# Performance work log

Hardware: AMD Instinct MI355X
Metric: run time of the kernel (lower is better)

## Reference

```python
import jax, jax.numpy as jnp
import numpy as np

NUM_GRAPHS = 512

def gcn_conv(x, src, dst, W, b, n):
    # x: [N, Fin], W: [Fin, Fout]. PyG GCNConv: add self loops, symmetric norm.
    h = x @ W  # [N, Fout]
    loop = jnp.arange(n)
    s = jnp.concatenate([src, loop])
    d = jnp.concatenate([dst, loop])
    ones = jnp.ones(s.shape[0], dtype=h.dtype)
    deg = jax.ops.segment_sum(ones, d, num_segments=n)  # includes self loop -> >= 1
    dinv = jax.lax.rsqrt(deg)
    norm = dinv[s] * dinv[d]  # [E+N]
    msg = h[s] * norm[:, None]  # gather + scale (memory-bound)
    out = jax.ops.segment_sum(msg, d, num_segments=n)
    return out + b

def setup_inputs() -> dict:
    key = jax.random.key(0)
    ks = jax.random.split(key, 10)
    N, E, F, H, O, EF = 100000, 1600000, 128, 128, 1, 16
    x = jax.random.normal(ks[0], (N, F), dtype=jnp.float32)
    edge_index = jax.random.randint(ks[1], (2, E), 0, N)
    edge_attr = jax.random.normal(ks[2], (E, EF), dtype=jnp.float32)
    batch = jnp.sort(jax.random.randint(ks[3], (N,), 0, NUM_GRAPHS))
    s1 = 1.0 / np.sqrt(F)
    s2 = 1.0 / np.sqrt(H)
    W1 = jax.random.uniform(ks[4], (F, H), jnp.float32, -s1, s1)
    b1 = jnp.zeros((H,), jnp.float32)
    W2 = jax.random.uniform(ks[5], (H, H), jnp.float32, -s2, s2)
    b2 = jnp.zeros((H,), jnp.float32)
    Wl = jax.random.uniform(ks[6], (H, O), jnp.float32, -s2, s2)
    bl = jnp.zeros((O,), jnp.float32)
    return {"x": x, "edge_index": edge_index, "edge_attr": edge_attr, "batch": batch,
            "W1": W1, "b1": b1, "W2": W2, "b2": b2, "Wl": Wl, "bl": bl}

def reference(x, edge_index, edge_attr, batch, W1, b1, W2, b2, Wl, bl):
    n = x.shape[0]
    src, dst = edge_index[0], edge_index[1]
    h = jax.nn.relu(gcn_conv(x, src, dst, W1, b1, n))
    h = gcn_conv(h, src, dst, W2, b2, n)
    # global mean pool by graph id
    summed = jax.ops.segment_sum(h, batch, num_segments=NUM_GRAPHS)  # [G, H]
    counts = jax.ops.segment_sum(jnp.ones((n,), h.dtype), batch, num_segments=NUM_GRAPHS)
    pooled = summed / jnp.maximum(counts, 1.0)[:, None]
    return pooled @ Wl + bl  # [G, 1]
```

## Files before the change

kernel.cpp:

```cpp
#include <hip/hip_runtime.h>


typedef __attribute__((ext_vector_type(8))) short short8;
typedef __attribute__((ext_vector_type(4))) float f32x4;

#define CHUNK 4096
#define RW    128
#define SCAP  6144
#define JCAP  512

__device__ __forceinline__ unsigned short bf16r(float f) {
    unsigned u = __float_as_uint(f);
    u += 0x7FFFu + ((u >> 16) & 1u);
    return (unsigned short)(u >> 16);
}

__device__ __forceinline__ float bff(unsigned short u) {
    return __uint_as_float((unsigned)u << 16);
}

__global__ void k_w1pack(const float* __restrict__ W1, unsigned short* __restrict__ w1p,
                         const float* __restrict__ W2, const float* __restrict__ Wl,
                         float* __restrict__ w2l) {
    if (blockIdx.x == 64) {
        int i = threadIdx.x;
        if (i < 128) {
            float s = 0.0f;
            for (int j = 0; j < 128; ++j) s = fmaf(W2[i * 128 + j], Wl[j], s);
            w2l[i] = s;
        }
        return;
    }
    int idx = blockIdx.x * 256 + threadIdx.x;
    int k = idx >> 7, n = idx & 127;
    w1p[((k >> 3) * 128 + n) * 8 + (k & 7)] = bf16r(W1[idx]);
}

__global__ __launch_bounds__(256) void k_part(
    const int* __restrict__ src, const int* __restrict__ dst,
    int* __restrict__ part, int* __restrict__ off_t, int* __restrict__ cnt_t,
    int E, int nchunks, int NR)
{
    __shared__ int stage[CHUNK];
    __shared__ int lcnt[1024];
    __shared__ int lscan[1024];
    int tid = threadIdx.x;
    int j = blockIdx.x;
    int base = j * CHUNK;

#pragma unroll
    for (int k = 0; k < 4; ++k) lcnt[tid + k * 256] = 0;
    __syncthreads();

    int mye[16], myr[16];
#pragma unroll
    for (int k = 0; k < 16; ++k) {
        int e = base + tid + (k << 8);
        bool ok = e < E;
        int s = ok ? src[e] : 0;
        int d = ok ? dst[e] : 0;
        int r = -1;
        if (ok) {
            r = d >> 7;
            atomicAdd(&lcnt[r], 1);
        }
        mye[k] = (s << 7) | (d & 127);
        myr[k] = r;
    }
    __syncthreads();

    int* pa = lcnt;
    int* pb = lscan;
    for (int off = 1; off < 1024; off <<= 1) {
#pragma unroll
        for (int k = 0; k < 4; ++k) {
            int idx = tid + k * 256;
            int v = pa[idx];
            if (idx >= off) v += pa[idx - off];
            pb[idx] = v;
        }
        __syncthreads();
        int* tmp = pa; pa = pb; pb = tmp;
    }
    for (int i = tid; i < NR; i += 256) {
        int incl = pa[i];
        int excl = (i == 0) ? 0 : pa[i - 1];
        pb[i] = excl;
        off_t[(size_t)i * nchunks + j] = excl;
        cnt_t[(size_t)i * nchunks + j] = incl - excl;
    }
    __syncthreads();

#pragma unroll
    for (int k = 0; k < 16; ++k) {
        if (myr[k] >= 0) {
            int p = atomicAdd(&pb[myr[k]], 1);
            stage[p] = mye[k];
        }
    }
    __syncthreads();

    int valid = E - base; if (valid > CHUNK) valid = CHUNK;
    for (int i = tid; i < valid; i += 256)
        part[(size_t)base + i] = stage[i];
}

__global__ __launch_bounds__(64) void k_rtot(
    const int* __restrict__ cnt_t, int* __restrict__ rtot, int nchunks)
{
    int r = blockIdx.x;
    int lane = threadIdx.x;
    const int* row = cnt_t + (size_t)r * nchunks;
    int s = 0;
    for (int j = lane; j < nchunks; j += 64) s += row[j];
#pragma unroll
    for (int off = 32; off > 0; off >>= 1) s += __shfl_xor(s, off);
    if (lane == 0) rtot[r] = s;
}

__global__ __launch_bounds__(1024) void k_rbase(
    const int* __restrict__ rtot, int* __restrict__ rbase, int NR)
{
    __shared__ int a1[1024], a2[1024];
    int tid = threadIdx.x;
    a1[tid] = (tid < NR) ? rtot[tid] : 0;
    __syncthreads();
    int* pa = a1; int* pb = a2;
    for (int off = 1; off < 1024; off <<= 1) {
        int v = pa[tid];
        if (tid >= off) v += pa[tid - off];
        pb[tid] = v;
        __syncthreads();
        int* tmp = pa; pa = pb; pb = tmp;
    }
    if (tid < NR) rbase[tid] = (tid == 0) ? 0 : pa[tid - 1];
    if (tid == 0) rbase[NR] = pa[NR >= 1 ? NR - 1 : 0];
}

__global__ __launch_bounds__(256) void k_rscat(
    const int* __restrict__ part, const int* __restrict__ off_t,
    const int* __restrict__ cnt_t, const int* __restrict__ rbase,
    int* __restrict__ srt, int* __restrict__ rp, float* __restrict__ dinv,
    int nchunks, int N, int E)
{
    __shared__ int stage[SCAP];
    __shared__ int jbase[JCAP];
    __shared__ int hist[RW], lcur[RW], s1[RW], s2[RW];
    __shared__ int cursor;
    int r = blockIdx.x;
    int tid = threadIdx.x;
    int d0 = r << 7;
    int width = N - d0; if (width > RW) width = RW;
    if (tid < RW) hist[tid] = 0;
    if (tid == 0) cursor = 0;
    __syncthreads();

    const int* orow = off_t + (size_t)r * nchunks;
    const int* crow = cnt_t + (size_t)r * nchunks;

    for (int j = tid; j < nchunks; j += 256) {
        int c = crow[j];
        if (c == 0) { if (j < JCAP) jbase[j] = 0; continue; }
        int b = (j < JCAP) ? atomicAdd(&cursor, c) : SCAP;
        if (j < JCAP) jbase[j] = b;
        const int* pp = part + (size_t)j * CHUNK + orow[j];
        for (int e = 0; e < c; ++e) {
            int ed = pp[e];
            int pos = b + e;
            if (pos < SCAP) stage[pos] = ed;
            atomicAdd(&hist[ed & 127], 1);
        }
    }
    __syncthreads();
    int total = cursor;

    if (tid < RW) s1[tid] = hist[tid];
    __syncthreads();
    int* pa = s1; int* pb = s2;
    for (int off = 1; off < RW; off <<= 1) {
        if (tid < RW) {
            int v = pa[tid];
            if (tid >= off) v += pa[tid - off];
            pb[tid] = v;
        }
        __syncthreads();
        int* tmp = pa; pa = pb; pb = tmp;
    }
    if (tid < width) {
        int excl = (tid == 0) ? 0 : pa[tid - 1];
        int start = rbase[r] + excl;
        rp[d0 + tid] = start;
        lcur[tid] = start;
        dinv[d0 + tid] = 1.0f / sqrtf((float)hist[tid] + 1.0f);
    }
    if (r == 0 && tid == 0) rp[N] = E;
    __syncthreads();

    int lim = total < SCAP ? total : SCAP;
    for (int i = tid; i < lim; i += 256) {
        int ed = stage[i];
        int pos = atomicAdd(&lcur[ed & 127], 1);
        srt[pos] = ed >> 7;
    }
    if (total > SCAP || nchunks > JCAP) {
        for (int j = tid; j < nchunks; j += 256) {
            int c = crow[j];
            if (c == 0) continue;
            int e0 = 0;
            if (j < JCAP) {
                int b = jbase[j];
                e0 = SCAP - b;
                if (e0 < 0) e0 = 0;
                if (e0 >= c) continue;
            }
            const int* pp = part + (size_t)j * CHUNK + orow[j];
            for (int e = e0; e < c; ++e) {
                int ed = pp[e];
                int pos = atomicAdd(&lcur[ed & 127], 1);
                srt[pos] = ed >> 7;
            }
        }
    }
}

__global__ __launch_bounds__(256) void k_mm_mfma(
    const float* __restrict__ A, const unsigned short* __restrict__ w1p,
    const float* __restrict__ dinv, unsigned short* __restrict__ C, int N)
{
    __shared__ unsigned short w1s[16384];
    int tid = threadIdx.x;
    {
        const uint4* s = (const uint4*)w1p;
        uint4* d = (uint4*)w1s;
#pragma unroll
        for (int i = 0; i < 8; ++i) d[tid + i * 256] = s[tid + i * 256];
    }
    __syncthreads();

    int w = tid >> 6, lane = tid & 63;
    int m = lane & 15, quad = lane >> 4;
    int r0 = blockIdx.x * 128 + w * 32;

    f32x4 acc[2][8];
#pragma unroll
    for (int rg = 0; rg < 2; ++rg)
#pragma unroll
        for (int cg = 0; cg < 8; ++cg) {
            f32x4 z = {0.0f, 0.0f, 0.0f, 0.0f};
            acc[rg][cg] = z;
        }

#pragma unroll
    for (int ks = 0; ks < 4; ++ks) {
        int k0 = ks * 32 + quad * 8;
        short8 a[2];
#pragma unroll
        for (int rg = 0; rg < 2; ++rg) {
            int r = r0 + rg * 16 + m;
            if (r > N - 1) r = N - 1;
            const float* ap = A + (size_t)r * 128 + k0;
            float4 v0 = *(const float4*)ap;
            float4 v1 = *(const float4*)(ap + 4);
            short8 av;
            av[0] = (short)bf16r(v0.x); av[1] = (short)bf16r(v0.y);
            av[2] = (short)bf16r(v0.z); av[3] = (short)bf16r(v0.w);
            av[4] = (short)bf16r(v1.x); av[5] = (short)bf16r(v1.y);
            av[6] = (short)bf16r(v1.z); av[7] = (short)bf16r(v1.w);
            a[rg] = av;
        }
        int kc = ks * 4 + quad;
#pragma unroll
        for (int cg = 0; cg < 8; ++cg) {
            const short8* bp = (const short8*)&w1s[((size_t)kc * 128 + cg * 16 + m) * 8];
            short8 b = *bp;
            acc[0][cg] = __builtin_amdgcn_mfma_f32_16x16x32_bf16(a[0], b, acc[0][cg], 0, 0, 0);
            acc[1][cg] = __builtin_amdgcn_mfma_f32_16x16x32_bf16(a[1], b, acc[1][cg], 0, 0, 0);
        }
    }

#pragma unroll
    for (int rg = 0; rg < 2; ++rg) {
        int rbase2 = r0 + rg * 16 + quad * 4;
#pragma unroll
        for (int reg = 0; reg < 4; ++reg) {
            int r = rbase2 + reg;
            if (r < N) {
                float s = dinv[r];
#pragma unroll
                for (int cg = 0; cg < 8; ++cg)
                    C[(size_t)r * 128 + cg * 16 + m] = bf16r(acc[rg][cg][reg] * s);
            }
        }
    }
}

__global__ __launch_bounds__(256) void k_agg1(
    const unsigned short* __restrict__ t, const float* __restrict__ dinv,
    const int* __restrict__ rp, const int* __restrict__ srt,
    const float* __restrict__ b1, const float* __restrict__ w2l,
    float* __restrict__ q, int N)
{
    __shared__ int shi[4][64];
    int wave = threadIdx.x >> 6;
    int lane = threadIdx.x & 63;
    int node = blockIdx.x * 4 + wave;
    if (node >= N) return;
    int s0 = rp[node], s1 = rp[node + 1];
    int deg = s1 - s0;
    int vdeg = deg < 63 ? deg : 63;

    int idx = N;
    if (lane < vdeg) idx = srt[s0 + lane];
    else if (lane == vdeg) idx = node;
    shi[wave][lane] = idx;
    const int* shw = shi[wave];

    int r4 = lane >> 4;
    int c = lane & 15;
    const unsigned short* tc = t + c * 8;

    float a[8];
#pragma unroll
    for (int k = 0; k < 8; ++k) a[k] = 0.0f;

    int nrows = vdeg + 1;
    int nquads = (nrows + 3) >> 2;
    int p = 0;
    do {
        short8 v[8];
#pragma unroll
        for (int j = 0; j < 8; ++j) {
            int id = shw[((p + j) << 2) + r4];
            v[j] = *(const short8*)(tc + (size_t)id * 128);
        }
#pragma unroll
        for (int j = 0; j < 8; ++j)
#pragma unroll
            for (int k = 0; k < 8; ++k)
                a[k] += bff((unsigned short)v[j][k]);
        p += 8;
    } while (p < nquads);

    if (deg > 63) {
        for (int e = s0 + 63; e < s1; ++e) {
            int id = srt[e];
            short8 v = *(const short8*)(tc + (size_t)id * 128);
            if (r4 == 0)
#pragma unroll
                for (int k = 0; k < 8; ++k)
                    a[k] += bff((unsigned short)v[k]);
        }
    }

#pragma unroll
    for (int k = 0; k < 8; ++k) {
        a[k] += __shfl_xor(a[k], 16);
        a[k] += __shfl_xor(a[k], 32);
    }

    float di = dinv[node];
    float4 b0 = *(const float4*)(b1 + c * 8);
    float4 b4 = *(const float4*)(b1 + c * 8 + 4);
    float4 w0 = *(const float4*)(w2l + c * 8);
    float4 w4 = *(const float4*)(w2l + c * 8 + 4);
    float pr = 0.0f;
    pr += fmaxf(fmaf(a[0], di, b0.x), 0.0f) * w0.x;
    pr += fmaxf(fmaf(a[1], di, b0.y), 0.0f) * w0.y;
    pr += fmaxf(fmaf(a[2], di, b0.z), 0.0f) * w0.z;
    pr += fmaxf(fmaf(a[3], di, b0.w), 0.0f) * w0.w;
    pr += fmaxf(fmaf(a[4], di, b4.x), 0.0f) * w4.x;
    pr += fmaxf(fmaf(a[5], di, b4.y), 0.0f) * w4.y;
    pr += fmaxf(fmaf(a[6], di, b4.z), 0.0f) * w4.z;
    pr += fmaxf(fmaf(a[7], di, b4.w), 0.0f) * w4.w;
#pragma unroll
    for (int off = 8; off > 0; off >>= 1) pr += __shfl_xor(pr, off);
    if (lane == 0) q[node] = pr * di;
}

__global__ __launch_bounds__(256) void k_agg2(
    const float* __restrict__ q, const float* __restrict__ dinv,
    const int* __restrict__ rp, const int* __restrict__ srt,
    float* __restrict__ p, int N)
{
    int tid = blockIdx.x * 256 + threadIdx.x;
    int node = tid >> 4;
    int l = tid & 15;
    if (node >= N) return;
    int s0 = rp[node], s1 = rp[node + 1];
    float a = 0.0f;
    for (int e = s0 + l; e < s1; e += 16) a += q[srt[e]];
#pragma unroll
    for (int off = 8; off > 0; off >>= 1) a += __shfl_xor(a, off);
    if (l == 0) p[node] = dinv[node] * (a + q[node]);
}

__global__ __launch_bounds__(64) void k_pool(
    const float* __restrict__ p, const int* __restrict__ batch,
    const float* __restrict__ b2, const float* __restrict__ Wl,
    const float* __restrict__ bl, float* __restrict__ out, int N, int G)
{
    int g = blockIdx.x;
    int lane = threadIdx.x;
    __shared__ int sb[2];
    if (lane < 2) {
        int target = g + lane;
        int lo = 0, hi = N;
        while (lo < hi) {
            int mid = (lo + hi) >> 1;
            if (batch[mid] < target) lo = mid + 1; else hi = mid;
        }
        sb[lane] = lo;
    }
    __syncthreads();
    int s = sb[0], e = sb[1];
    float a = 0.0f;
    for (int i = s + lane; i < e; i += 64) a += p[i];
#pragma unroll
    for (int off = 32; off > 0; off >>= 1) a += __shfl_xor(a, off);
    if (lane == 0) {
        float c = 0.0f;
        for (int j = 0; j < 128; ++j) c = fmaf(b2[j], Wl[j], c);
        out[g] = a / fmaxf((float)(e - s), 1.0f) + c + bl[0];
    }
}

extern "C" void kernel_launch(void* const* d_in, const int* in_sizes, int n_in,
                              void* d_out, int out_size, void* d_ws, size_t ws_size,
                              hipStream_t stream)
{
    const float* x  = (const float*)d_in[0];
    const int*   ei = (const int*)d_in[1];
    const int*   batch = (const int*)d_in[3];
    const float* W1 = (const float*)d_in[4];
    const float* b1 = (const float*)d_in[5];
    const float* W2 = (const float*)d_in[6];
    const float* b2 = (const float*)d_in[7];
    const float* Wl = (const float*)d_in[8];
    const float* bl = (const float*)d_in[9];

    int N = in_sizes[0] / 128;
    int E = in_sizes[1] / 2;
    const int* src = ei;
    const int* dst = ei + E;

    char* ws = (char*)d_ws;
    size_t off = 0;
    auto alloc = [&](size_t bytes) -> void* {
        void* p = ws + off;
        off = (off + bytes + 255) & ~(size_t)255;
        return p;
    };
    int nchunks = (E + CHUNK - 1) / CHUNK;
    int NR = (N + RW - 1) / RW;
    unsigned short* t = (unsigned short*)alloc((size_t)(N + 1) * 128 * 2);
    float* q    = (float*)alloc((size_t)N * 4);
    float* p    = (float*)alloc((size_t)N * 4);
    int*   srt  = (int*)alloc((size_t)E * 4);
    int*   part = (int*)alloc((size_t)nchunks * CHUNK * 4);
    int*   off_t= (int*)alloc((size_t)NR * nchunks * 4);
    int*   cnt_t= (int*)alloc((size_t)NR * nchunks * 4);
    int*   rtot = (int*)alloc((size_t)NR * 4);
    int*   rbase= (int*)alloc((size_t)(NR + 1) * 4);
    float* dinv = (float*)alloc((size_t)N * 4);
    int*   rp   = (int*)alloc((size_t)(N + 1) * 4);
    float* w2l  = (float*)alloc(128 * 4);
    unsigned short* w1p = (unsigned short*)alloc(16384 * 2);
    (void)ws_size;

    hipMemsetAsync(t + (size_t)N * 128, 0, 256, stream);

    k_part<<<nchunks, 256, 0, stream>>>(src, dst, part, off_t, cnt_t, E, nchunks, NR);
    k_w1pack<<<65, 256, 0, stream>>>(W1, w1p, W2, Wl, w2l);
    k_rtot<<<NR, 64, 0, stream>>>(cnt_t, rtot, nchunks);
    k_rbase<<<1, 1024, 0, stream>>>(rtot, rbase, NR);
    k_rscat<<<NR, 256, 0, stream>>>(part, off_t, cnt_t, rbase, srt, rp, dinv,
                                    nchunks, N, E);

    int mmb = (N + 127) / 128;
    k_mm_mfma<<<mmb, 256, 0, stream>>>(x, w1p, dinv, t, N);
    k_agg1<<<(N + 3) / 4, 256, 0, stream>>>(t, dinv, rp, srt, b1, w2l, q, N);
    k_agg2<<<((size_t)N * 16 + 255) / 256, 256, 0, stream>>>(q, dinv, rp, srt, p, N);
    k_pool<<<512, 64, 0, stream>>>(p, batch, b2, Wl, bl, (float*)d_out, N, 512);
}
```

Measured before the change: 337.9 us.

## Make agg1 persistent with prefetched next-node neighbor indices in double-buffered LDS

The first aggregation kernel becomes a grid-stride persistent kernel with 2048 blocks, so each wave processes many nodes instead of one. While it gathers the current node's rows, it loads the next node's row pointers, dinv value and neighbor indices, and stores them in a second LDS buffer. The goal is to hide the index-load latency and cut per-wave launch and setup cost, and bias/weight loads are hoisted out of the loop. In exchange it uses more registers, and the fixed grid size may reduce occupancy or balance load less well.

```diff
diff --git a/kernel.cpp b/kernel.cpp
--- a/kernel.cpp
+++ b/kernel.cpp
@@ -298,83 +298,108 @@
     const unsigned short* __restrict__ t, const float* __restrict__ dinv,
     const int* __restrict__ rp, const int* __restrict__ srt,
     const float* __restrict__ b1, const float* __restrict__ w2l,
-    float* __restrict__ q, int N)
-{
-    __shared__ int shi[4][64];
+    float* __restrict__ q, int N, int nwaves)
+{
+    __shared__ int shi[4][2][64];
     int wave = threadIdx.x >> 6;
     int lane = threadIdx.x & 63;
-    int node = blockIdx.x * 4 + wave;
-    if (node >= N) return;
-    int s0 = rp[node], s1 = rp[node + 1];
-    int deg = s1 - s0;
-    int vdeg = deg < 63 ? deg : 63;
-
-    int idx = N;
-    if (lane < vdeg) idx = srt[s0 + lane];
-    else if (lane == vdeg) idx = node;
-    shi[wave][lane] = idx;
-    const int* shw = shi[wave];
+    int gw = blockIdx.x * 4 + wave;
+    if (gw >= N) return;
 
     int r4 = lane >> 4;
     int c = lane & 15;
     const unsigned short* tc = t + c * 8;
 
-    float a[8];
-#pragma unroll
-    for (int k = 0; k < 8; ++k) a[k] = 0.0f;
-
-    int nrows = vdeg + 1;
-    int nquads = (nrows + 3) >> 2;
-    int p = 0;
-    do {
-        short8 v[8];
-#pragma unroll
-        for (int j = 0; j < 8; ++j) {
-            int id = shw[((p + j) << 2) + r4];
-            v[j] = *(const short8*)(tc + (size_t)id * 128);
-        }
-#pragma unroll
-        for (int j = 0; j < 8; ++j)
-#pragma unroll
-            for (int k = 0; k < 8; ++k)
-                a[k] += bff((unsigned short)v[j][k]);
-        p += 8;
-    } while (p < nquads);
-
-    if (deg > 63) {
-        for (int e = s0 + 63; e < s1; ++e) {
-            int id = srt[e];
-            short8 v = *(const short8*)(tc + (size_t)id * 128);
-            if (r4 == 0)
-#pragma unroll
-                for (int k = 0; k < 8; ++k)
-                    a[k] += bff((unsigned short)v[k]);
-        }
-    }
-
-#pragma unroll
-    for (int k = 0; k < 8; ++k) {
-        a[k] += __shfl_xor(a[k], 16);
-        a[k] += __shfl_xor(a[k], 32);
-    }
-
-    float di = dinv[node];
     float4 b0 = *(const float4*)(b1 + c * 8);
     float4 b4 = *(const float4*)(b1 + c * 8 + 4);
     float4 w0 = *(const float4*)(w2l + c * 8);
     float4 w4 = *(const float4*)(w2l + c * 8 + 4);
-    float pr = 0.0f;
-    pr += fmaxf(fmaf(a[0], di, b0.x), 0.0f) * w0.x;
-    pr += fmaxf(fmaf(a[1], di, b0.y), 0.0f) * w0.y;
-    pr += fmaxf(fmaf(a[2], di, b0.z), 0.0f) * w0.z;
-    pr += fmaxf(fmaf(a[3], di, b0.w), 0.0f) * w0.w;
-    pr += fmaxf(fmaf(a[4], di, b4.x), 0.0f) * w4.x;
-    pr += fmaxf(fmaf(a[5], di, b4.y), 0.0f) * w4.y;
-    pr += fmaxf(fmaf(a[6], di, b4.z), 0.0f) * w4.z;
-    pr += fmaxf(fmaf(a[7], di, b4.w), 0.0f) * w4.w;
-#pragma unroll
-    for (int off = 8; off > 0; off >>= 1) pr += __shfl_xor(pr, off);
-    if (lane == 0) q[node] = pr * di;
+
+    int node = gw;
+    int s0 = rp[node], s1 = rp[node + 1];
+    float di = dinv[node];
+    {
+        int deg = s1 - s0;
+        int vdeg = deg < 63 ? deg : 63;
+        int idx = N;
+        if (lane < vdeg) idx = srt[s0 + lane];
+        else if (lane == vdeg) idx = node;
+        shi[wave][0][lane] = idx;
+    }
+    int buf = 0;
+
+    while (true) {
+        int nnode = node + nwaves;
+        int ns0 = 0, ns1 = 0, nidx = N;
+        float ndi = 0.0f;
+        bool have_next = nnode < N;
+        if (have_next) {
+            ns0 = rp[nnode]; ns1 = rp[nnode + 1];
+            ndi = dinv[nnode];
+            int ndeg = ns1 - ns0;
+            int nvdeg = ndeg < 63 ? ndeg : 63;
+            if (lane < nvdeg) nidx = srt[ns0 + lane];
+            else if (lane == nvdeg) nidx = nnode;
+        }
+
+        const int* shw = shi[wave][buf];
+        int deg = s1 - s0;
+        int vdeg = deg < 63 ? deg : 63;
+        float a[8];
+#pragma unroll
+        for (int k = 0; k < 8; ++k) a[k] = 0.0f;
+        int nrows = vdeg + 1;
+        int nquads = (nrows + 3) >> 2;
+        int p = 0;
+        do {
+            short8 v[8];
+#pragma unroll
+            for (int j = 0; j < 8; ++j) {
+                int id = shw[((p + j) << 2) + r4];
+                v[j] = *(const short8*)(tc + (size_t)id * 128);
+            }
+#pragma unroll
+            for (int j = 0; j < 8; ++j)
+#pragma unroll
+                for (int k = 0; k < 8; ++k)
+                    a[k] += bff((unsigned short)v[j][k]);
+            p += 8;
+        } while (p < nquads);
+
+        if (deg > 63) {
+            for (int e = s0 + 63; e < s1; ++e) {
+                int id = srt[e];
+                short8 v = *(const short8*)(tc + (size_t)id * 128);
+                if (r4 == 0)
+#pragma unroll
+                    for (int k = 0; k < 8; ++k)
+                        a[k] += bff((unsigned short)v[k]);
+            }
+        }
+
+#pragma unroll
+        for (int k = 0; k < 8; ++k) {
+            a[k] += __shfl_xor(a[k], 16);
+            a[k] += __shfl_xor(a[k], 32);
+        }
+
+        float pr = 0.0f;
+        pr += fmaxf(fmaf(a[0], di, b0.x), 0.0f) * w0.x;
+        pr += fmaxf(fmaf(a[1], di, b0.y), 0.0f) * w0.y;
+        pr += fmaxf(fmaf(a[2], di, b0.z), 0.0f) * w0.z;
+        pr += fmaxf(fmaf(a[3], di, b0.w), 0.0f) * w0.w;
+        pr += fmaxf(fmaf(a[4], di, b4.x), 0.0f) * w4.x;
+        pr += fmaxf(fmaf(a[5], di, b4.y), 0.0f) * w4.y;
+        pr += fmaxf(fmaf(a[6], di, b4.z), 0.0f) * w4.z;
+        pr += fmaxf(fmaf(a[7], di, b4.w), 0.0f) * w4.w;
+#pragma unroll
+        for (int off = 8; off > 0; off >>= 1) pr += __shfl_xor(pr, off);
+        if (lane == 0) q[node] = pr * di;
+
+        if (!have_next) break;
+        shi[wave][buf ^ 1][lane] = nidx;
+        node = nnode; s0 = ns0; s1 = ns1; di = ndi; buf ^= 1;
+    }
 }
 
 __global__ __launch_bounds__(256) void k_agg2(
@@ -478,7 +503,8 @@
 
     int mmb = (N + 127) / 128;
     k_mm_mfma<<<mmb, 256, 0, stream>>>(x, w1p, dinv, t, N);
-    k_agg1<<<(N + 3) / 4, 256, 0, stream>>>(t, dinv, rp, srt, b1, w2l, q, N);
+    int a1b = 2048;
+    k_agg1<<<a1b, 256, 0, stream>>>(t, dinv, rp, srt, b1, w2l, q, N, a1b * 4);
     k_agg2<<<((size_t)N * 16 + 255) / 256, 256, 0, stream>>>(q, dinv, rp, srt, p, N);
     k_pool<<<512, 64, 0, stream>>>(p, batch, b2, Wl, bl, (float*)d_out, N, 512);
 }
```

Measured after the change: 336.1 us. About the same (-0.6%).
